# Kernel tuning notes

Hardware: AMD Instinct MI355X
Metric: run time of the kernel (lower is better)

## Reference

```python
import jax, jax.numpy as jnp
import numpy as np
import math

N, T, D, H = 8, 1024, 768, 12

def setup_inputs() -> dict:
    key = jax.random.key(0)
    ks = jax.random.split(key, 5)
    s = 1.0 / math.sqrt(D)
    return {
        "x": jax.random.normal(ks[0], (N, T, D), dtype=jnp.float32),
        "Wq": jax.random.normal(ks[1], (D, D), dtype=jnp.float32) * s,
        "Wk": jax.random.normal(ks[2], (D, D), dtype=jnp.float32) * s,
        "Wv": jax.random.normal(ks[3], (D, D), dtype=jnp.float32) * s,
        "Wo": jax.random.normal(ks[4], (D, D), dtype=jnp.float32) * s,
        "bo": jnp.zeros((D,), dtype=jnp.float32),
    }

def reference(x, Wq, Wk, Wv, Wo, bo):
    n, t, d = x.shape
    h = H
    dh = d // h  # 64
    # nn.Linear: y = x @ W.T
    q = (x @ Wq.T).reshape(n, t, h, dh).transpose(0, 2, 1, 3)  # [n,h,t,dh]
    k = (x @ Wk.T).reshape(n, t, h, dh).transpose(0, 2, 1, 3)
    v = (x @ Wv.T).reshape(n, t, h, dh).transpose(0, 2, 1, 3)
    scores = jnp.einsum('nhqd,nhkd->nhqk', q, k) / math.sqrt(dh)  # [n,h,t,t]
    causal = jnp.tril(jnp.ones((t, t), dtype=bool))
    scores = jnp.where(causal, scores, -jnp.inf)
    attn = jax.nn.softmax(scores, axis=-1)
    out = jnp.einsum('nhqk,nhkd->nhqd', attn, v)  # [n,h,t,dh]
    out = out.transpose(0, 2, 1, 3).reshape(n, t, d)
    return out @ Wo.T + bo
```

## Files before the change

### kernel.cpp

```cpp
#include <hip/hip_runtime.h>

typedef __attribute__((ext_vector_type(8))) short short8;
typedef __attribute__((ext_vector_type(4))) float f32x4;
typedef __attribute__((ext_vector_type(4))) short short4v;
typedef __attribute__((ext_vector_type(4))) unsigned short ushort4v;

#define DEV static __device__ __forceinline__

DEV unsigned short f2bf(float f) {
  unsigned int u = __builtin_bit_cast(unsigned int, f);
  u += 0x7fffu + ((u >> 16) & 1u);
  return (unsigned short)(u >> 16);
}

DEV unsigned int pack2bf(float a, float b) {
  return (unsigned int)f2bf(a) | ((unsigned int)f2bf(b) << 16);
}

DEV void gload16(const void* g, void* l) {
  __builtin_amdgcn_global_load_lds(
      (const __attribute__((address_space(1))) unsigned int*)g,
      (__attribute__((address_space(3))) unsigned int*)l, 16, 0, 0);
}

__global__ __launch_bounds__(256) void cvt_bf16(const float* __restrict__ in,
                                                unsigned short* __restrict__ out,
                                                int nvec4) {
  int i = blockIdx.x * 256 + threadIdx.x;
  if (i >= nvec4) return;
  float4 v = ((const float4*)in)[i];
  ushort4v o = {f2bf(v.x), f2bf(v.y), f2bf(v.z), f2bf(v.w)};
  *(ushort4v*)(out + (size_t)i * 4) = o;
}

__global__ __launch_bounds__(256) void cvt_w4(const float* __restrict__ w0,
                                              const float* __restrict__ w1,
                                              const float* __restrict__ w2,
                                              const float* __restrict__ w3,
                                              unsigned short* __restrict__ out) {
  int i = blockIdx.x * 256 + threadIdx.x;
  int wsel = i / 147456;
  int j = i - wsel * 147456;
  const float* src = wsel == 0 ? w0 : wsel == 1 ? w1 : wsel == 2 ? w2 : w3;
  float4 v = ((const float4*)src)[j];
  ushort4v o = {f2bf(v.x), f2bf(v.y), f2bf(v.z), f2bf(v.w)};
  *(ushort4v*)(out + (size_t)i * 4) = o;
}

__global__ __launch_bounds__(256) void gemm_qkv(const short* __restrict__ A,
                                                const short* __restrict__ B0,
                                                unsigned short* __restrict__ QK,
                                                unsigned short* __restrict__ Vt) {
  __shared__ short As[2][128 * 32];
  __shared__ short Bs[2][128 * 32];
  const int tid = threadIdx.x;
  const int lane = tid & 63;
  const int wave = tid >> 6;
  const int row0 = blockIdx.x * 128;
  const int wsel = blockIdx.y / 6;
  const int col0 = (blockIdx.y % 6) * 128;
  const short* B = B0 + (size_t)wsel * 589824;
  const int wr = (wave >> 1) * 64;
  const int wc = (wave & 1) * 64;

  f32x4 acc[4][4] = {};

  const short* aG = A + (size_t)(row0 + wave * 16 + (lane >> 2)) * 768 + (lane & 3) * 8;
  const short* bG = B + (size_t)(col0 + wave * 16 + (lane >> 2)) * 768 + (lane & 3) * 8;
  char* aL = (char*)&As[0][0] + wave * 1024;
  char* bL = (char*)&Bs[0][0] + wave * 1024;

  const int cl = lane & 15;
  const int g8 = (lane >> 4) * 8;

#define QKV_STAGE(buf, kk)                          \
  do {                                              \
    gload16(aG + (kk), aL + (buf)*8192);            \
    gload16(aG + 64 * 768 + (kk), aL + (buf)*8192 + 4096); \
    gload16(bG + (kk), bL + (buf)*8192);            \
    gload16(bG + 64 * 768 + (kk), bL + (buf)*8192 + 4096); \
  } while (0)

#define QKV_COMPUTE(buf)                                                          \
  do {                                                                            \
    short8 af[4], bfr[4];                                                         \
    _Pragma("unroll") for (int m = 0; m < 4; m++)                                 \
        af[m] = *(const short8*)&As[buf][(wr + m * 16 + cl) * 32 + g8];           \
    _Pragma("unroll") for (int n = 0; n < 4; n++)                                 \
        bfr[n] = *(const short8*)&Bs[buf][(wc + n * 16 + cl) * 32 + g8];          \
    _Pragma("unroll") for (int m = 0; m < 4; m++)                                 \
        _Pragma("unroll") for (int n = 0; n < 4; n++)                             \
            acc[m][n] = __builtin_amdgcn_mfma_f32_16x16x32_bf16(af[m], bfr[n],    \
                                                                acc[m][n], 0, 0, 0); \
  } while (0)

  QKV_STAGE(0, 0);
  __syncthreads();
  int cur = 0;
  for (int kk = 32; kk < 768; kk += 32) {
    QKV_STAGE(cur ^ 1, kk);
    QKV_COMPUTE(cur);
    __syncthreads();
    cur ^= 1;
  }
  QKV_COMPUTE(cur);

  const int r4 = (lane >> 4) * 4;
  unsigned short* Qout = QK + (size_t)wsel * 6291456;
#pragma unroll
  for (int m = 0; m < 4; m++) {
#pragma unroll
    for (int n = 0; n < 4; n++) {
      const int row = row0 + wr + m * 16 + r4;
      const int col = col0 + wc + n * 16 + cl;
      if (wsel < 2) {
#pragma unroll
        for (int r = 0; r < 4; r++) {
          Qout[(size_t)(((((row + r) >> 10) * 12 + (col >> 6)) << 16) +
                        (((row + r) & 1023) << 6) + (col & 63))] = f2bf(acc[m][n][r]);
        }
      } else {
        short4v ov;
#pragma unroll
        for (int r = 0; r < 4; r++) ov[r] = (short)f2bf(acc[m][n][r]);
        *(short4v*)((short*)Vt + (size_t)((((row >> 10) * 12 + (col >> 6)) << 16) +
                                          ((col & 63) << 10) + (row & 1023))) = ov;
      }
    }
  }
}

__global__ __launch_bounds__(256) void gemm_out(const short* __restrict__ A,
                                                const short* __restrict__ B,
                                                float* __restrict__ Cout,
                                                const float* __restrict__ bias) {
  __shared__ short As[2][128 * 32];
  __shared__ short Bs[2][128 * 32];
  const int tid = threadIdx.x;
  const int lane = tid & 63;
  const int wave = tid >> 6;
  const int row0 = blockIdx.x * 128;
  const int col0 = blockIdx.y * 128;
  const int wr = (wave >> 1) * 64;
  const int wc = (wave & 1) * 64;

  f32x4 acc[4][4] = {};

  const short* aG = A + (size_t)(row0 + wave * 16 + (lane >> 2)) * 768 + (lane & 3) * 8;
  const short* bG = B + (size_t)(col0 + wave * 16 + (lane >> 2)) * 768 + (lane & 3) * 8;
  char* aL = (char*)&As[0][0] + wave * 1024;
  char* bL = (char*)&Bs[0][0] + wave * 1024;

  const int cl = lane & 15;
  const int g8 = (lane >> 4) * 8;

  QKV_STAGE(0, 0);
  __syncthreads();
  int cur = 0;
  for (int kk = 32; kk < 768; kk += 32) {
    QKV_STAGE(cur ^ 1, kk);
    QKV_COMPUTE(cur);
    __syncthreads();
    cur ^= 1;
  }
  QKV_COMPUTE(cur);

  const int r4 = (lane >> 4) * 4;
#pragma unroll
  for (int m = 0; m < 4; m++) {
#pragma unroll
    for (int n = 0; n < 4; n++) {
#pragma unroll
      for (int r = 0; r < 4; r++) {
        const int row = row0 + wr + m * 16 + r4 + r;
        const int col = col0 + wc + n * 16 + cl;
        Cout[(size_t)row * 768 + col] = acc[m][n][r] + bias[col];
      }
    }
  }
}

__global__ __launch_bounds__(512) void attn_fwd(const short* __restrict__ Qh,
                                                const short* __restrict__ Kh,
                                                const short* __restrict__ Vt,
                                                short* __restrict__ Obuf) {
  __shared__ short Ks[2][32 * 72];
  __shared__ short Vs[2][64 * 40];
  __shared__ unsigned int Ps[8][16 * 36];

  const int tid = threadIdx.x;
  const int lane = tid & 63;
  const int wave = tid >> 6;
  const int w4 = wave & 3;
  const int gg = wave >> 2;
  const int t8 = tid & 255;
  const int nh = blockIdx.y;
  const int nIdx = nh / 12;
  const int hIdx = nh % 12;
  const int hb = nh << 16;
  const int qloc = lane & 15;
  const int g = lane >> 4;
  const int kRow = t8 >> 3, kColB = (t8 & 7) * 8;
  const int vRow = t8 >> 2, vColB = (t8 & 3) * 8;
  short* KsG = &Ks[gg][0];
  short* VsG = &Vs[gg][0];
  float* Mbuf = (float*)&Ps[0][0];
  float* slot = Mbuf + (size_t)(w4 * 64 + lane) * 18;

  const float SCL = 0.18033688f;

  for (int p = 0; p < 2; p++) {
    const int qb = p ? (15 - (int)blockIdx.x) : (int)blockIdx.x;
    const int nsteps = qb + 1;
    const int qr0 = qb * 64 + w4 * 16;
    const int qg = qr0 + qloc;
    const int qmax = qr0 + 15;

    short8 qf[2];
    qf[0] = *(const short8*)&Qh[hb + qg * 64 + g * 8];
    qf[1] = *(const short8*)&Qh[hb + qg * 64 + 32 + g * 8];

    float m_run = -INFINITY, l_run = 0.f;
    f32x4 o[4] = {};

    for (int s = 0; s < nsteps; s++) {
      const int kv0 = (s + gg * nsteps) * 32;
      *(short8*)&KsG[kRow * 72 + kColB] = *(const short8*)&Kh[hb + (kv0 + kRow) * 64 + kColB];
      *(short8*)&VsG[vRow * 40 + vColB] = *(const short8*)&Vt[hb + vRow * 1024 + kv0 + vColB];
      __syncthreads();
      if (kv0 <= qmax) {
        f32x4 s2[2] = {};
#pragma unroll
        for (int c = 0; c < 2; c++) {
          short8 a0 = *(const short8*)&KsG[qloc * 72 + c * 32 + g * 8];
          short8 a1 = *(const short8*)&KsG[(16 + qloc) * 72 + c * 32 + g * 8];
          s2[0] = __builtin_amdgcn_mfma_f32_16x16x32_bf16(a0, qf[c], s2[0], 0, 0, 0);
          s2[1] = __builtin_amdgcn_mfma_f32_16x16x32_bf16(a1, qf[c], s2[1], 0, 0, 0);
        }
        float pv[2][4];
        float pm = -INFINITY;
        if (kv0 + 31 <= qr0) {
#pragma unroll
          for (int kt = 0; kt < 2; kt++)
#pragma unroll
            for (int r = 0; r < 4; r++) {
              float sv = s2[kt][r] * SCL;
              pv[kt][r] = sv;
              pm = fmaxf(pm, sv);
            }
        } else {
#pragma unroll
          for (int kt = 0; kt < 2; kt++)
#pragma unroll
            for (int r = 0; r < 4; r++) {
              const int kg = kv0 + kt * 16 + g * 4 + r;
              float sv = s2[kt][r] * SCL;
              sv = (kg <= qg) ? sv : -INFINITY;
              pv[kt][r] = sv;
              pm = fmaxf(pm, sv);
            }
        }
        pm = fmaxf(pm, __shfl_xor(pm, 16));
        pm = fmaxf(pm, __shfl_xor(pm, 32));
        if (__all(pm <= m_run + 11.5f)) {
          float lsum = 0.f;
#pragma unroll
          for (int kt = 0; kt < 2; kt++)
#pragma unroll
            for (int r = 0; r < 4; r++) {
              float pp = exp2f(pv[kt][r] - m_run);
              pv[kt][r] = pp;
              lsum += pp;
            }
          lsum += __shfl_xor(lsum, 16);
          lsum += __shfl_xor(lsum, 32);
          l_run += lsum;
        } else {
          const float mnew = fmaxf(m_run, pm);
          const float corr = exp2f(m_run - mnew);
          float lsum = 0.f;
#pragma unroll
          for (int kt = 0; kt < 2; kt++)
#pragma unroll
            for (int r = 0; r < 4; r++) {
              float pp = exp2f(pv[kt][r] - mnew);
              pv[kt][r] = pp;
              lsum += pp;
            }
          lsum += __shfl_xor(lsum, 16);
          lsum += __shfl_xor(lsum, 32);
          l_run = l_run * corr + lsum;
          m_run = mnew;
#pragma unroll
          for (int dt = 0; dt < 4; dt++) o[dt] *= corr;
        }
        unsigned int* pr = &Ps[wave][qloc * 36];
#pragma unroll
        for (int kt = 0; kt < 2; kt++) {
          pr[kt * 8 + g * 2] = pack2bf(pv[kt][0], pv[kt][1]);
          pr[kt * 8 + g * 2 + 1] = pack2bf(pv[kt][2], pv[kt][3]);
        }
        __asm__ volatile("" ::: "memory");
        short8 pf = *(const short8*)((const short*)&Ps[wave][0] + qloc * 72 + g * 8);
#pragma unroll
        for (int dt = 0; dt < 4; dt++) {
          short8 vf = *(const short8*)&VsG[(dt * 16 + qloc) * 40 + g * 8];
          o[dt] = __builtin_amdgcn_mfma_f32_16x16x32_bf16(vf, pf, o[dt], 0, 0, 0);
        }
      }
      __syncthreads();
    }

    if (gg == 1) {
#pragma unroll
      for (int dt = 0; dt < 4; dt++)
#pragma unroll
        for (int r = 0; r < 4; r++) slot[dt * 4 + r] = o[dt][r];
      slot[16] = m_run;
      slot[17] = l_run;
    }
    __syncthreads();
    if (gg == 0) {
      const float m1 = slot[16], l1 = slot[17];
      const float mm = fmaxf(m_run, m1);
      const float c0 = exp2f(m_run - mm);
      const float c1 = exp2f(m1 - mm);
      const float inv = 1.f / (l_run * c0 + l1 * c1);
      const int outRow = nIdx * 1024 + qr0 + qloc;
      short* op = Obuf + (size_t)outRow * 768 + hIdx * 64;
#pragma unroll
      for (int dt = 0; dt < 4; dt++) {
        short4v ov;
#pragma unroll
        for (int r = 0; r < 4; r++)
          ov[r] = (short)f2bf((o[dt][r] * c0 + slot[dt * 4 + r] * c1) * inv);
        *(short4v*)(op + dt * 16 + g * 4) = ov;
      }
    }
    __syncthreads();
  }
}

extern "C" void kernel_launch(void* const* d_in, const int* in_sizes, int n_in,
                              void* d_out, int out_size, void* d_ws, size_t ws_size,
                              hipStream_t stream) {
  (void)in_sizes; (void)n_in; (void)out_size; (void)ws_size;
  const float* x  = (const float*)d_in[0];
  const float* Wq = (const float*)d_in[1];
  const float* Wk = (const float*)d_in[2];
  const float* Wv = (const float*)d_in[3];
  const float* Wo = (const float*)d_in[4];
  const float* bo = (const float*)d_in[5];

  char* ws = (char*)d_ws;
  short* xb  = (short*)(ws);
  short* wqb = (short*)(ws + 12582912);
  short* wob = (short*)(ws + 12582912 + 3 * 1179648);
  short* Qh  = (short*)(ws + 17301504);
  short* Kh  = (short*)(ws + 17301504 + 12582912);
  short* Vt  = (short*)(ws + 17301504 + 2 * 12582912);
  short* Ob  = (short*)(ws + 17301504 + 3 * 12582912);

  cvt_bf16<<<6144, 256, 0, stream>>>(x, (unsigned short*)xb, 1572864);
  cvt_w4<<<2304, 256, 0, stream>>>(Wq, Wk, Wv, Wo, (unsigned short*)wqb);

  gemm_qkv<<<dim3(64, 18), 256, 0, stream>>>(xb, wqb, (unsigned short*)Qh,
                                             (unsigned short*)Vt);

  attn_fwd<<<dim3(8, 96), 512, 0, stream>>>(Qh, Kh, Vt, Ob);

  gemm_out<<<dim3(64, 6), 256, 0, stream>>>(Ob, wob, (float*)d_out, bo);
}
```

Before: 210.1 us.

## Replace split-KV two-group attention with single-group register-prefetched double-buffered loop

```diff
diff --git a/kernel.cpp b/kernel.cpp
--- a/kernel.cpp
+++ b/kernel.cpp
@@ -180,39 +180,34 @@
   }
 }
 
-__global__ __launch_bounds__(512) void attn_fwd(const short* __restrict__ Qh,
+__global__ __launch_bounds__(256) void attn_fwd(const short* __restrict__ Qh,
                                                 const short* __restrict__ Kh,
                                                 const short* __restrict__ Vt,
                                                 short* __restrict__ Obuf) {
   __shared__ short Ks[2][32 * 72];
   __shared__ short Vs[2][64 * 40];
-  __shared__ unsigned int Ps[8][16 * 36];
+  __shared__ unsigned int Ps[4][16 * 36];
 
   const int tid = threadIdx.x;
   const int lane = tid & 63;
-  const int wave = tid >> 6;
-  const int w4 = wave & 3;
-  const int gg = wave >> 2;
-  const int t8 = tid & 255;
-  const int nh = blockIdx.y;
+  const int w = tid >> 6;
+  const int bid = blockIdx.x;
+  const int nh = (bid & 7) * 12 + ((bid >> 3) % 12);
+  const int pr = (bid >> 3) / 12;
   const int nIdx = nh / 12;
   const int hIdx = nh % 12;
   const int hb = nh << 16;
   const int qloc = lane & 15;
   const int g = lane >> 4;
-  const int kRow = t8 >> 3, kColB = (t8 & 7) * 8;
-  const int vRow = t8 >> 2, vColB = (t8 & 3) * 8;
-  short* KsG = &Ks[gg][0];
-  short* VsG = &Vs[gg][0];
-  float* Mbuf = (float*)&Ps[0][0];
-  float* slot = Mbuf + (size_t)(w4 * 64 + lane) * 18;
+  const int kRow = tid >> 3, kColB = (tid & 7) * 8;
+  const int vRow = tid >> 2, vColB = (tid & 3) * 8;
 
   const float SCL = 0.18033688f;
 
   for (int p = 0; p < 2; p++) {
-    const int qb = p ? (15 - (int)blockIdx.x) : (int)blockIdx.x;
-    const int nsteps = qb + 1;
-    const int qr0 = qb * 64 + w4 * 16;
+    const int qb = p ? (15 - pr) : pr;
+    const int nsteps = 2 * qb + 2;
+    const int qr0 = qb * 64 + w * 16;
     const int qg = qr0 + qloc;
     const int qmax = qr0 + 15;
 
@@ -220,20 +215,29 @@
     qf[0] = *(const short8*)&Qh[hb + qg * 64 + g * 8];
     qf[1] = *(const short8*)&Qh[hb + qg * 64 + 32 + g * 8];
 
-    float m_run = -INFINITY, l_run = 0.f;
+    float m_run = -INFINITY, l_lane = 0.f;
     f32x4 o[4] = {};
 
+    short8 krg = *(const short8*)&Kh[hb + kRow * 64 + kColB];
+    short8 vrg = *(const short8*)&Vt[hb + vRow * 1024 + vColB];
+    int buf = 0;
+
     for (int s = 0; s < nsteps; s++) {
-      const int kv0 = (s + gg * nsteps) * 32;
-      *(short8*)&KsG[kRow * 72 + kColB] = *(const short8*)&Kh[hb + (kv0 + kRow) * 64 + kColB];
-      *(short8*)&VsG[vRow * 40 + vColB] = *(const short8*)&Vt[hb + vRow * 1024 + kv0 + vColB];
+      const int kv0 = s * 32;
+      *(short8*)&Ks[buf][kRow * 72 + kColB] = krg;
+      *(short8*)&Vs[buf][vRow * 40 + vColB] = vrg;
       __syncthreads();
+      if (s + 1 < nsteps) {
+        const int kn = kv0 + 32;
+        krg = *(const short8*)&Kh[hb + (kn + kRow) * 64 + kColB];
+        vrg = *(const short8*)&Vt[hb + vRow * 1024 + kn + vColB];
+      }
       if (kv0 <= qmax) {
         f32x4 s2[2] = {};
 #pragma unroll
         for (int c = 0; c < 2; c++) {
-          short8 a0 = *(const short8*)&KsG[qloc * 72 + c * 32 + g * 8];
-          short8 a1 = *(const short8*)&KsG[(16 + qloc) * 72 + c * 32 + g * 8];
+          short8 a0 = *(const short8*)&Ks[buf][qloc * 72 + c * 32 + g * 8];
+          short8 a1 = *(const short8*)&Ks[buf][(16 + qloc) * 72 + c * 32 + g * 8];
           s2[0] = __builtin_amdgcn_mfma_f32_16x16x32_bf16(a0, qf[c], s2[0], 0, 0, 0);
           s2[1] = __builtin_amdgcn_mfma_f32_16x16x32_bf16(a1, qf[c], s2[1], 0, 0, 0);
         }
@@ -263,81 +267,63 @@
         pm = fmaxf(pm, __shfl_xor(pm, 16));
         pm = fmaxf(pm, __shfl_xor(pm, 32));
         if (__all(pm <= m_run + 11.5f)) {
-          float lsum = 0.f;
+          float ls = 0.f;
 #pragma unroll
           for (int kt = 0; kt < 2; kt++)
 #pragma unroll
             for (int r = 0; r < 4; r++) {
               float pp = exp2f(pv[kt][r] - m_run);
               pv[kt][r] = pp;
-              lsum += pp;
+              ls += pp;
             }
-          lsum += __shfl_xor(lsum, 16);
-          lsum += __shfl_xor(lsum, 32);
-          l_run += lsum;
+          l_lane += ls;
         } else {
           const float mnew = fmaxf(m_run, pm);
           const float corr = exp2f(m_run - mnew);
-          float lsum = 0.f;
+          float ls = 0.f;
 #pragma unroll
           for (int kt = 0; kt < 2; kt++)
 #pragma unroll
             for (int r = 0; r < 4; r++) {
               float pp = exp2f(pv[kt][r] - mnew);
               pv[kt][r] = pp;
-              lsum += pp;
+              ls += pp;
             }
-          lsum += __shfl_xor(lsum, 16);
-          lsum += __shfl_xor(lsum, 32);
-          l_run = l_run * corr + lsum;
+          l_lane = l_lane * corr + ls;
           m_run = mnew;
 #pragma unroll
           for (int dt = 0; dt < 4; dt++) o[dt] *= corr;
         }
-        unsigned int* pr = &Ps[wave][qloc * 36];
+        unsigned int* pp_ = &Ps[w][qloc * 36];
 #pragma unroll
         for (int kt = 0; kt < 2; kt++) {
-          pr[kt * 8 + g * 2] = pack2bf(pv[kt][0], pv[kt][1]);
-          pr[kt * 8 + g * 2 + 1] = pack2bf(pv[kt][2], pv[kt][3]);
+          pp_[kt * 8 + g * 2] = pack2bf(pv[kt][0], pv[kt][1]);
+          pp_[kt * 8 + g * 2 + 1] = pack2bf(pv[kt][2], pv[kt][3]);
         }
         __asm__ volatile("" ::: "memory");
-        short8 pf = *(const short8*)((const short*)&Ps[wave][0] + qloc * 72 + g * 8);
+        short8 pf = *(const short8*)((const short*)&Ps[w][0] + qloc * 72 + g * 8);
 #pragma unroll
         for (int dt = 0; dt < 4; dt++) {
-          short8 vf = *(const short8*)&VsG[(dt * 16 + qloc) * 40 + g * 8];
+          short8 vf = *(const short8*)&Vs[buf][(dt * 16 + qloc) * 40 + g * 8];
           o[dt] = __builtin_amdgcn_mfma_f32_16x16x32_bf16(vf, pf, o[dt], 0, 0, 0);
         }
       }
       __syncthreads();
+      buf ^= 1;
     }
 
-    if (gg == 1) {
-#pragma unroll
-      for (int dt = 0; dt < 4; dt++)
-#pragma unroll
-        for (int r = 0; r < 4; r++) slot[dt * 4 + r] = o[dt][r];
-      slot[16] = m_run;
-      slot[17] = l_run;
+    float l_tot = l_lane + __shfl_xor(l_lane, 16);
+    l_tot += __shfl_xor(l_tot, 32);
+    const float inv = 1.f / l_tot;
+    const int outRow = nIdx * 1024 + qr0 + qloc;
+    short* op = Obuf + (size_t)outRow * 768 + hIdx * 64;
+#pragma unroll
+    for (int dt = 0; dt < 4; dt++) {
+      short4v ov;
+#pragma unroll
+      for (int r = 0; r < 4; r++) ov[r] = (short)f2bf(o[dt][r] * inv);
+      *(short4v*)(op + dt * 16 + g * 4) = ov;
     }
-    __syncthreads();
-    if (gg == 0) {
-      const float m1 = slot[16], l1 = slot[17];
-      const float mm = fmaxf(m_run, m1);
-      const float c0 = exp2f(m_run - mm);
-      const float c1 = exp2f(m1 - mm);
-      const float inv = 1.f / (l_run * c0 + l1 * c1);
-      const int outRow = nIdx * 1024 + qr0 + qloc;
-      short* op = Obuf + (size_t)outRow * 768 + hIdx * 64;
-#pragma unroll
-      for (int dt = 0; dt < 4; dt++) {
-        short4v ov;
-#pragma unroll
-        for (int r = 0; r < 4; r++)
-          ov[r] = (short)f2bf((o[dt][r] * c0 + slot[dt * 4 + r] * c1) * inv);
-        *(short4v*)(op + dt * 16 + g * 4) = ov;
-      }
-    }
-    __syncthreads();
   }
 }
 
@@ -367,7 +353,7 @@
   gemm_qkv<<<dim3(64, 18), 256, 0, stream>>>(xb, wqb, (unsigned short*)Qh,
                                              (unsigned short*)Vt);
 
-  attn_fwd<<<dim3(8, 96), 512, 0, stream>>>(Qh, Kh, Vt, Ob);
+  attn_fwd<<<768, 256, 0, stream>>>(Qh, Kh, Vt, Ob);
 
   gemm_out<<<dim3(64, 6), 256, 0, stream>>>(Ob, wob, (float*)d_out, bo);
 }
```

Result: faster. 201.5 us (-4.1%).
